# Kernel tuning notes

Hardware: AMD Instinct MI355X
Metric: run time of the kernel (lower is better)

The kernel has to match this reference:

```python
import jax, jax.numpy as jnp
import numpy as np

# config values (from init_kwargs)
TRANSFORM_PENALTY = 0.5
EXACT_MATCH_BONUS = 5.0
ULTRA_TEAL_IOU = 0.85
STRICT_MATCH_W = 0.15
CREATIVITY_W = 0.1
STRATEGIC_W = 0.1
MULTI_STEP_W = 0.1
GAMMA = 2.5
NUM_COLORS = 10


def setup_inputs() -> dict:
    key = jax.random.key(0)
    ks = jax.random.split(key, 6)
    B, C, H, W = 2048, 10, 48, 48
    return {
        "pred": jax.random.normal(ks[0], (B, C, H, W), dtype=jnp.float32),
        "strategic_features": jax.random.normal(ks[1], (B, 256), dtype=jnp.float32),
        "planning_score": jax.random.uniform(ks[2], (B,), dtype=jnp.float32),
        "reasoning_depth": jax.random.uniform(ks[3], (B,), dtype=jnp.float32),
        "targets": jax.random.randint(ks[4], (B, H, W), 0, 10, dtype=jnp.int32),
        "inputs": jax.random.randint(ks[5], (B, H, W), 0, 10, dtype=jnp.int32),
    }


def _spatial_weights(H, W, dtype):
    # weight = 1 + 0.3 * (1 - dist_from_center / max_dist), computed analytically
    cy, cx = H // 2, W // 2
    yy = jnp.arange(H, dtype=dtype)[:, None]
    xx = jnp.arange(W, dtype=dtype)[None, :]
    dist = jnp.sqrt((yy - cy) ** 2 + (xx - cx) ** 2)
    max_dist = np.sqrt((H // 2) ** 2 + (W // 2) ** 2)
    return 1.0 + 0.3 * (1.0 - dist / max_dist)  # [H, W]


def reference(pred, strategic_features, planning_score, reasoning_depth, targets, inputs):
    B, C, H, W = pred.shape
    t = targets  # label smoothing followed by argmax recovers the original indices

    # ---- enhanced strategic focal loss ----
    logp = jax.nn.log_softmax(pred, axis=1)                         # [B,C,H,W]
    ce = -jnp.take_along_axis(logp, t[:, None, :, :], axis=1)[:, 0]  # [B,H,W]
    pt = jnp.exp(-ce)
    # per-batch unique-color count (fixed small C -> loop over classes is fine)
    present = jnp.stack([jnp.any(t == c, axis=(1, 2)) for c in range(C)], axis=-1)  # [B,C]
    unique_colors = present.sum(axis=-1)                             # [B]
    # per-batch color-transition count (horizontal + vertical)
    transitions = (t[:, :, 1:] != t[:, :, :-1]).sum(axis=(1, 2)) + \
                  (t[:, 1:, :] != t[:, :-1, :]).sum(axis=(1, 2))     # [B]
    w = jnp.where(unique_colors > 4, 1.3, 1.0) * jnp.where(transitions > W, 1.2, 1.0)
    focal = jnp.mean((1.0 - pt) ** GAMMA * ce * w[:, None, None])

    # ---- ultra-teal weighted IoU + strict matches ----
    pred_idx = jnp.argmax(pred, axis=1)                              # [B,H,W]
    eq = (pred_idx == t)
    strict = jnp.all(eq, axis=(1, 2)).astype(pred.dtype)             # [B]
    sw = _spatial_weights(H, W, pred.dtype)                          # [H,W]
    weighted_iou = (eq.astype(pred.dtype) * sw).sum(axis=(1, 2)) / sw.sum()
    ultra_teal = ULTRA_TEAL_IOU * weighted_iou + STRICT_MATCH_W * strict
    exact_bonus = jnp.maximum(-ultra_teal.mean() * EXACT_MATCH_BONUS, -5.0)

    # ---- copy (transform) penalty ----
    copy = jnp.all(pred_idx == inputs, axis=(1, 2)).astype(pred.dtype)
    transform_penalty = copy.mean() * TRANSFORM_PENALTY

    # ---- optional bonuses ----
    creativity_bonus = jax.nn.sigmoid(strategic_features.mean()) * CREATIVITY_W
    strategic_bonus = planning_score.mean() * STRATEGIC_W
    multi_step_bonus = reasoning_depth.mean() * MULTI_STEP_W
    complexity_bonus = ultra_teal.mean() * (H * W / 1225.0) * 0.1    # H > 20 (static)

    total = (focal + transform_penalty + exact_bonus
             - creativity_bonus - strategic_bonus - multi_step_bonus - complexity_bonus)
    total = jnp.where(jnp.isnan(total) | jnp.isinf(total), jnp.minimum(focal, 10.0), total)
    return total
```

## Files before the change

### kernel.cpp

```cpp
#include <hip/hip_runtime.h>
#include <math.h>

#define BB 2048
#define CC 10
#define HH 48
#define WW 48
#define HWSZ (HH * WW)
#define HW4 (HWSZ / 4)
#define NTHREADS 256

__device__ __forceinline__ float wave_sum_f(float v) {
    #pragma unroll
    for (int off = 32; off > 0; off >>= 1) v += __shfl_down(v, off, 64);
    return v;
}
__device__ __forceinline__ int wave_sum_i(int v) {
    #pragma unroll
    for (int off = 32; off > 0; off >>= 1) v += __shfl_down(v, off, 64);
    return v;
}
__device__ __forceinline__ int wave_or_i(int v) {
    #pragma unroll
    for (int off = 32; off > 0; off >>= 1) v |= __shfl_down(v, off, 64);
    return v;
}

__global__ __launch_bounds__(NTHREADS) void per_batch_kernel(
    const float* __restrict__ pred,
    const float* __restrict__ sfeat,
    const int*   __restrict__ targets,
    const int*   __restrict__ inputs,
    float* __restrict__ focal_ws,
    float* __restrict__ ultra_teal_o,
    float* __restrict__ copy_o,
    float* __restrict__ sf_sum_o)
{
    __shared__ int tgt[HWSZ];
    __shared__ float rf[4][4];
    __shared__ int ri[4][4];

    const int b = blockIdx.x;
    const int tid = threadIdx.x;

    const float4* __restrict__ pb4 = (const float4*)(pred + (size_t)b * CC * HWSZ);
    const int4*   __restrict__ tb4 = (const int4*)(targets + (size_t)b * HWSZ);
    const int4*   __restrict__ ib4 = (const int4*)(inputs + (size_t)b * HWSZ);

    for (int g = tid; g < HW4; g += NTHREADS) {
        ((int4*)tgt)[g] = tb4[g];
    }
    __syncthreads();

    float focal_f = 0.f, iou_f = 0.f, sw_f = 0.f;
    int eq_cnt = 0, copy_cnt = 0, trans_cnt = 0, mask = 0;

    const float sw_scale = 0.3f / 33.9411254969543f;

    for (int g = tid; g < HW4; g += NTHREADS) {
        float chv[CC][4];
        #pragma unroll
        for (int c = 0; c < CC; ++c) {
            float4 v = pb4[c * HW4 + g];
            chv[c][0] = v.x; chv[c][1] = v.y; chv[c][2] = v.z; chv[c][3] = v.w;
        }
        int4 t4 = ((const int4*)tgt)[g];
        int4 i4 = ib4[g];
        int tj[4] = {t4.x, t4.y, t4.z, t4.w};
        int ij[4] = {i4.x, i4.y, i4.z, i4.w};

        const int y  = g / (WW / 4);
        const int x0 = (g % (WW / 4)) * 4;
        const int p0 = y * WW + x0;
        const float dy = (float)(y - 24);
        const float dy2 = dy * dy;

        #pragma unroll
        for (int j = 0; j < 4; ++j) {
            const int t = tj[j];
            mask |= (1 << t);
            const int x = x0 + j;
            if (x < WW - 1) trans_cnt += (t != tgt[p0 + j + 1]);
            if (y < HH - 1) trans_cnt += (t != tgt[p0 + j + WW]);

            float m = chv[0][j];
            int am = 0;
            float vt = (t == 0) ? chv[0][j] : 0.f;
            #pragma unroll
            for (int c = 1; c < CC; ++c) {
                float vv = chv[c][j];
                if (vv > m) { m = vv; am = c; }
                if (c == t) vt = vv;
            }
            float s = 0.f;
            #pragma unroll
            for (int c = 0; c < CC; ++c) s += __expf(chv[c][j] - m);
            const float lse = m + __logf(s);
            const float logpt = vt - lse;
            const float ce = -logpt;
            const float pt = __expf(logpt);
            const float om = fmaxf(1.f - pt, 0.f);
            focal_f += __powf(om, 2.5f) * ce;

            const bool e = (am == t);
            eq_cnt  += e;
            copy_cnt += (am == ij[j]);
            const float dx = (float)(x - 24);
            const float sw = 1.3f - sw_scale * __fsqrt_rn(dy2 + dx * dx);
            sw_f += sw;
            if (e) iou_f += sw;
        }
    }

    float sf = sfeat[(size_t)b * 256 + tid];

    focal_f = wave_sum_f(focal_f);
    iou_f   = wave_sum_f(iou_f);
    sw_f    = wave_sum_f(sw_f);
    sf      = wave_sum_f(sf);
    eq_cnt  = wave_sum_i(eq_cnt);
    copy_cnt= wave_sum_i(copy_cnt);
    trans_cnt = wave_sum_i(trans_cnt);
    mask    = wave_or_i(mask);

    const int wv = tid >> 6;
    if ((tid & 63) == 0) {
        rf[0][wv] = focal_f; rf[1][wv] = iou_f; rf[2][wv] = sw_f; rf[3][wv] = sf;
        ri[0][wv] = eq_cnt;  ri[1][wv] = copy_cnt; ri[2][wv] = trans_cnt; ri[3][wv] = mask;
    }
    __syncthreads();
    if (tid == 0) {
        float F = 0.f, I = 0.f, S = 0.f, SF = 0.f;
        int EQ = 0, CP = 0, TR = 0, MK = 0;
        #pragma unroll
        for (int i = 0; i < 4; ++i) {
            F += rf[0][i]; I += rf[1][i]; S += rf[2][i]; SF += rf[3][i];
            EQ += ri[0][i]; CP += ri[1][i]; TR += ri[2][i]; MK |= ri[3][i];
        }
        const int uniq = __popc(MK);
        const float w = ((uniq > 4) ? 1.3f : 1.0f) * ((TR > WW) ? 1.2f : 1.0f);
        const float strict = (EQ == HWSZ) ? 1.f : 0.f;
        const float ut = 0.85f * (I / S) + 0.15f * strict;
        focal_ws[b]    = F * w;
        ultra_teal_o[b] = ut;
        copy_o[b]      = (CP == HWSZ) ? 1.f : 0.f;
        sf_sum_o[b]    = SF;
    }
}

__global__ __launch_bounds__(NTHREADS) void finalize_kernel(
    const float* __restrict__ focal_ws,
    const float* __restrict__ ultra_teal,
    const float* __restrict__ copy_v,
    const float* __restrict__ sf_sum,
    const float* __restrict__ planning,
    const float* __restrict__ reasoning,
    float* __restrict__ out)
{
    __shared__ float rf[6][4];
    const int tid = threadIdx.x;
    float f = 0.f, u = 0.f, c = 0.f, s = 0.f, p = 0.f, r = 0.f;
    for (int i = tid; i < BB; i += NTHREADS) {
        f += focal_ws[i];
        u += ultra_teal[i];
        c += copy_v[i];
        s += sf_sum[i];
        p += planning[i];
        r += reasoning[i];
    }
    f = wave_sum_f(f); u = wave_sum_f(u); c = wave_sum_f(c);
    s = wave_sum_f(s); p = wave_sum_f(p); r = wave_sum_f(r);
    const int wv = tid >> 6;
    if ((tid & 63) == 0) {
        rf[0][wv] = f; rf[1][wv] = u; rf[2][wv] = c;
        rf[3][wv] = s; rf[4][wv] = p; rf[5][wv] = r;
    }
    __syncthreads();
    if (tid == 0) {
        float F = 0.f, U = 0.f, Cv = 0.f, S = 0.f, P = 0.f, R = 0.f;
        #pragma unroll
        for (int i = 0; i < 4; ++i) {
            F += rf[0][i]; U += rf[1][i]; Cv += rf[2][i];
            S += rf[3][i]; P += rf[4][i]; R += rf[5][i];
        }
        const float focal = F / (float)(BB * HWSZ);
        const float ut_mean = U / (float)BB;
        const float exact_bonus = fmaxf(-ut_mean * 5.0f, -5.0f);
        const float transform_penalty = (Cv / (float)BB) * 0.5f;
        const float sf_mean = S / (float)(BB * 256);
        const float creativity = (1.0f / (1.0f + __expf(-sf_mean))) * 0.1f;
        const float strategic = (P / (float)BB) * 0.1f;
        const float multi = (R / (float)BB) * 0.1f;
        const float complexity = ut_mean * ((float)HWSZ / 1225.0f) * 0.1f;
        float total = focal + transform_penalty + exact_bonus
                    - creativity - strategic - multi - complexity;
        if (isnan(total) || isinf(total)) total = fminf(focal, 10.0f);
        out[0] = total;
    }
}

extern "C" void kernel_launch(void* const* d_in, const int* in_sizes, int n_in,
                              void* d_out, int out_size, void* d_ws, size_t ws_size,
                              hipStream_t stream) {
    const float* pred      = (const float*)d_in[0];
    const float* sfeat     = (const float*)d_in[1];
    const float* planning  = (const float*)d_in[2];
    const float* reasoning = (const float*)d_in[3];
    const int*   targets   = (const int*)d_in[4];
    const int*   inputs    = (const int*)d_in[5];
    float* out = (float*)d_out;

    float* ws = (float*)d_ws;
    float* focal_ws   = ws;
    float* ultra_teal = ws + BB;
    float* copy_v     = ws + 2 * BB;
    float* sf_sum     = ws + 3 * BB;

    per_batch_kernel<<<BB, NTHREADS, 0, stream>>>(
        pred, sfeat, targets, inputs, focal_ws, ultra_teal, copy_v, sf_sum);
    finalize_kernel<<<1, NTHREADS, 0, stream>>>(
        focal_ws, ultra_teal, copy_v, sf_sum, planning, reasoning, out);
}
```

Measured before the change: 303.7 us.

## Rework per-batch kernel to 384 threads with float2 loads and unrolled iterations

The per-batch block grows from 256 to 384 threads, and each thread processes 2 pixels per step instead of 4, with a fully unrolled fixed trip count (3 iterations). Targets and inputs are prefetched into registers, spatial weights are precomputed into shared memory, and pow(om,2.5) becomes om*om*sqrt(om). The aim is more independent memory loads in flight and less per-pixel math on this memory-bound kernel. The trade-off is narrower 8-byte loads, which may issue more instructions per byte, plus extra shared memory and register pressure.

```diff
diff --git a/kernel.cpp b/kernel.cpp
--- a/kernel.cpp
+++ b/kernel.cpp
@@ -6,8 +6,10 @@
 #define HH 48
 #define WW 48
 #define HWSZ (HH * WW)
-#define HW4 (HWSZ / 4)
-#define NTHREADS 256
+#define HW2 (HWSZ / 2)
+#define NT 384
+#define NITER (HW2 / NT)
+#define NWAVE (NT / 64)
 
 __device__ __forceinline__ float wave_sum_f(float v) {
     #pragma unroll
@@ -25,7 +27,7 @@
     return v;
 }
 
-__global__ __launch_bounds__(NTHREADS) void per_batch_kernel(
+__global__ __launch_bounds__(NT, 4) void per_batch_kernel(
     const float* __restrict__ pred,
     const float* __restrict__ sfeat,
     const int*   __restrict__ targets,
@@ -35,96 +37,114 @@
     float* __restrict__ copy_o,
     float* __restrict__ sf_sum_o)
 {
-    __shared__ int tgt[HWSZ];
-    __shared__ float rf[4][4];
-    __shared__ int ri[4][4];
+    __shared__ int   tgt[HWSZ];
+    __shared__ float swt[HWSZ];
+    __shared__ float rf[4][NWAVE];
+    __shared__ int   ri[4][NWAVE];
 
     const int b = blockIdx.x;
     const int tid = threadIdx.x;
 
-    const float4* __restrict__ pb4 = (const float4*)(pred + (size_t)b * CC * HWSZ);
-    const int4*   __restrict__ tb4 = (const int4*)(targets + (size_t)b * HWSZ);
-    const int4*   __restrict__ ib4 = (const int4*)(inputs + (size_t)b * HWSZ);
-
-    for (int g = tid; g < HW4; g += NTHREADS) {
-        ((int4*)tgt)[g] = tb4[g];
+    const float2* __restrict__ pb2 = (const float2*)(pred + (size_t)b * CC * HWSZ);
+    const int2*   __restrict__ tb2 = (const int2*)(targets + (size_t)b * HWSZ);
+    const int2*   __restrict__ ib2 = (const int2*)(inputs + (size_t)b * HWSZ);
+
+    int2 treg[NITER], ireg[NITER];
+    #pragma unroll
+    for (int k = 0; k < NITER; ++k) {
+        const int g = tid + k * NT;
+        treg[k] = tb2[g];
+        ireg[k] = ib2[g];
+        ((int2*)tgt)[g] = treg[k];
+    }
+    const float sw_scale = 0.3f / 33.9411254969543f;
+    #pragma unroll
+    for (int k = 0; k < HWSZ / NT; ++k) {
+        const int s = tid + k * NT;
+        const int y = s / WW;
+        const int x = s - y * WW;
+        const float dy = (float)(y - 24);
+        const float dx = (float)(x - 24);
+        swt[s] = 1.3f - sw_scale * __fsqrt_rn(dy * dy + dx * dx);
     }
     __syncthreads();
 
-    float focal_f = 0.f, iou_f = 0.f, sw_f = 0.f;
+    float focal_f = 0.f, iou_f = 0.f, swsum_f = 0.f;
     int eq_cnt = 0, copy_cnt = 0, trans_cnt = 0, mask = 0;
 
-    const float sw_scale = 0.3f / 33.9411254969543f;
-
-    for (int g = tid; g < HW4; g += NTHREADS) {
-        float chv[CC][4];
+    #pragma unroll
+    for (int k = 0; k < NITER; ++k) {
+        const int g = tid + k * NT;
+        float2 v[CC];
+        #pragma unroll
+        for (int c = 0; c < CC; ++c) v[c] = pb2[c * HW2 + g];
+
+        const int2 t2 = treg[k];
+        const int2 i2 = ireg[k];
+        const int p0 = 2 * g;
+        const int y  = g / (WW / 2);
+        const int x0 = (g - y * (WW / 2)) * 2;
+
+        int th = (t2.x != t2.y);
+        if (x0 < WW - 2) th += (t2.y != tgt[p0 + 2]);
+        if (y < HH - 1) {
+            const int2 bl = ((const int2*)tgt)[g + WW / 2];
+            th += (t2.x != bl.x) + (t2.y != bl.y);
+        }
+        trans_cnt += th;
+        mask |= (1 << t2.x) | (1 << t2.y);
+
+        float m0 = v[0].x, m1 = v[0].y;
+        int a0 = 0, a1 = 0;
+        float vt0 = (t2.x == 0) ? v[0].x : 0.f;
+        float vt1 = (t2.y == 0) ? v[0].y : 0.f;
+        #pragma unroll
+        for (int c = 1; c < CC; ++c) {
+            const float vx = v[c].x, vy = v[c].y;
+            if (vx > m0) { m0 = vx; a0 = c; }
+            if (vy > m1) { m1 = vy; a1 = c; }
+            if (c == t2.x) vt0 = vx;
+            if (c == t2.y) vt1 = vy;
+        }
+        float s0 = 0.f, s1 = 0.f;
         #pragma unroll
         for (int c = 0; c < CC; ++c) {
-            float4 v = pb4[c * HW4 + g];
-            chv[c][0] = v.x; chv[c][1] = v.y; chv[c][2] = v.z; chv[c][3] = v.w;
-        }
-        int4 t4 = ((const int4*)tgt)[g];
-        int4 i4 = ib4[g];
-        int tj[4] = {t4.x, t4.y, t4.z, t4.w};
-        int ij[4] = {i4.x, i4.y, i4.z, i4.w};
-
-        const int y  = g / (WW / 4);
-        const int x0 = (g % (WW / 4)) * 4;
-        const int p0 = y * WW + x0;
-        const float dy = (float)(y - 24);
-        const float dy2 = dy * dy;
-
-        #pragma unroll
-        for (int j = 0; j < 4; ++j) {
-            const int t = tj[j];
-            mask |= (1 << t);
-            const int x = x0 + j;
-            if (x < WW - 1) trans_cnt += (t != tgt[p0 + j + 1]);
-            if (y < HH - 1) trans_cnt += (t != tgt[p0 + j + WW]);
-
-            float m = chv[0][j];
-            int am = 0;
-            float vt = (t == 0) ? chv[0][j] : 0.f;
-            #pragma unroll
-            for (int c = 1; c < CC; ++c) {
-                float vv = chv[c][j];
-                if (vv > m) { m = vv; am = c; }
-                if (c == t) vt = vv;
-            }
-            float s = 0.f;
-            #pragma unroll
-            for (int c = 0; c < CC; ++c) s += __expf(chv[c][j] - m);
-            const float lse = m + __logf(s);
-            const float logpt = vt - lse;
-            const float ce = -logpt;
-            const float pt = __expf(logpt);
-            const float om = fmaxf(1.f - pt, 0.f);
-            focal_f += __powf(om, 2.5f) * ce;
-
-            const bool e = (am == t);
-            eq_cnt  += e;
-            copy_cnt += (am == ij[j]);
-            const float dx = (float)(x - 24);
-            const float sw = 1.3f - sw_scale * __fsqrt_rn(dy2 + dx * dx);
-            sw_f += sw;
-            if (e) iou_f += sw;
-        }
-    }
-
-    float sf = sfeat[(size_t)b * 256 + tid];
-
-    focal_f = wave_sum_f(focal_f);
-    iou_f   = wave_sum_f(iou_f);
-    sw_f    = wave_sum_f(sw_f);
-    sf      = wave_sum_f(sf);
-    eq_cnt  = wave_sum_i(eq_cnt);
-    copy_cnt= wave_sum_i(copy_cnt);
+            s0 += __expf(v[c].x - m0);
+            s1 += __expf(v[c].y - m1);
+        }
+        const float lse0 = m0 + __logf(s0);
+        const float lse1 = m1 + __logf(s1);
+        const float ce0 = lse0 - vt0;
+        const float ce1 = lse1 - vt1;
+        const float pt0 = __expf(vt0 - lse0);
+        const float pt1 = __expf(vt1 - lse1);
+        const float om0 = fmaxf(1.f - pt0, 0.f);
+        const float om1 = fmaxf(1.f - pt1, 0.f);
+        focal_f += om0 * om0 * __fsqrt_rn(om0) * ce0
+                 + om1 * om1 * __fsqrt_rn(om1) * ce1;
+
+        eq_cnt   += (a0 == t2.x) + (a1 == t2.y);
+        copy_cnt += (a0 == i2.x) + (a1 == i2.y);
+
+        const float2 swp = ((const float2*)swt)[g];
+        swsum_f += swp.x + swp.y;
+        iou_f   += ((a0 == t2.x) ? swp.x : 0.f) + ((a1 == t2.y) ? swp.y : 0.f);
+    }
+
+    float sf = (tid < 256) ? sfeat[(size_t)b * 256 + tid] : 0.f;
+
+    focal_f  = wave_sum_f(focal_f);
+    iou_f    = wave_sum_f(iou_f);
+    swsum_f  = wave_sum_f(swsum_f);
+    sf       = wave_sum_f(sf);
+    eq_cnt   = wave_sum_i(eq_cnt);
+    copy_cnt = wave_sum_i(copy_cnt);
     trans_cnt = wave_sum_i(trans_cnt);
-    mask    = wave_or_i(mask);
+    mask     = wave_or_i(mask);
 
     const int wv = tid >> 6;
     if ((tid & 63) == 0) {
-        rf[0][wv] = focal_f; rf[1][wv] = iou_f; rf[2][wv] = sw_f; rf[3][wv] = sf;
+        rf[0][wv] = focal_f; rf[1][wv] = iou_f; rf[2][wv] = swsum_f; rf[3][wv] = sf;
         ri[0][wv] = eq_cnt;  ri[1][wv] = copy_cnt; ri[2][wv] = trans_cnt; ri[3][wv] = mask;
     }
     __syncthreads();
@@ -132,7 +152,7 @@
         float F = 0.f, I = 0.f, S = 0.f, SF = 0.f;
         int EQ = 0, CP = 0, TR = 0, MK = 0;
         #pragma unroll
-        for (int i = 0; i < 4; ++i) {
+        for (int i = 0; i < NWAVE; ++i) {
             F += rf[0][i]; I += rf[1][i]; S += rf[2][i]; SF += rf[3][i];
             EQ += ri[0][i]; CP += ri[1][i]; TR += ri[2][i]; MK |= ri[3][i];
         }
@@ -140,14 +160,14 @@
         const float w = ((uniq > 4) ? 1.3f : 1.0f) * ((TR > WW) ? 1.2f : 1.0f);
         const float strict = (EQ == HWSZ) ? 1.f : 0.f;
         const float ut = 0.85f * (I / S) + 0.15f * strict;
-        focal_ws[b]    = F * w;
+        focal_ws[b]     = F * w;
         ultra_teal_o[b] = ut;
-        copy_o[b]      = (CP == HWSZ) ? 1.f : 0.f;
-        sf_sum_o[b]    = SF;
-    }
-}
-
-__global__ __launch_bounds__(NTHREADS) void finalize_kernel(
+        copy_o[b]       = (CP == HWSZ) ? 1.f : 0.f;
+        sf_sum_o[b]     = SF;
+    }
+}
+
+__global__ __launch_bounds__(256) void finalize_kernel(
     const float* __restrict__ focal_ws,
     const float* __restrict__ ultra_teal,
     const float* __restrict__ copy_v,
@@ -159,7 +179,7 @@
     __shared__ float rf[6][4];
     const int tid = threadIdx.x;
     float f = 0.f, u = 0.f, c = 0.f, s = 0.f, p = 0.f, r = 0.f;
-    for (int i = tid; i < BB; i += NTHREADS) {
+    for (int i = tid; i < BB; i += 256) {
         f += focal_ws[i];
         u += ultra_teal[i];
         c += copy_v[i];
@@ -215,8 +235,8 @@
     float* copy_v     = ws + 2 * BB;
     float* sf_sum     = ws + 3 * BB;
 
-    per_batch_kernel<<<BB, NTHREADS, 0, stream>>>(
+    per_batch_kernel<<<BB, NT, 0, stream>>>(
         pred, sfeat, targets, inputs, focal_ws, ultra_teal, copy_v, sf_sum);
-    finalize_kernel<<<1, NTHREADS, 0, stream>>>(
+    finalize_kernel<<<1, 256, 0, stream>>>(
         focal_ws, ultra_teal, copy_v, sf_sum, planning, reasoning, out);
 }
```

New measurement: 296.8 us. -2.3%, faster.

## Split each batch image across three blocks with one float4 group per thread

Applied to the files above, without the earlier changes.

Each batch item is now handled by three blocks of 192 threads. Each thread loads exactly one float4 group of all ten channels up front, instead of one 256-thread block looping over 576 groups. The per-batch weighting (unique colours, transitions, strict match) moves into a 1024-thread finalize kernel that combines the three partial records per batch. This raises the number of blocks and the memory-level parallelism, and replaces powf with om*om*sqrt(om). The cost is a larger intermediate workspace and a heavier single-block finalize.

```diff
diff --git a/kernel.cpp b/kernel.cpp
--- a/kernel.cpp
+++ b/kernel.cpp
@@ -7,7 +7,10 @@
 #define WW 48
 #define HWSZ (HH * WW)
 #define HW4 (HWSZ / 4)
-#define NTHREADS 256
+#define NPART 3
+#define NT1 192
+#define GPP (HW4 / NPART)
+#define NFLD 8
 
 __device__ __forceinline__ float wave_sum_f(float v) {
     #pragma unroll
@@ -25,171 +28,181 @@
     return v;
 }
 
-__global__ __launch_bounds__(NTHREADS) void per_batch_kernel(
+__global__ __launch_bounds__(NT1) void part_kernel(
     const float* __restrict__ pred,
     const float* __restrict__ sfeat,
     const int*   __restrict__ targets,
     const int*   __restrict__ inputs,
-    float* __restrict__ focal_ws,
-    float* __restrict__ ultra_teal_o,
-    float* __restrict__ copy_o,
-    float* __restrict__ sf_sum_o)
+    float* __restrict__ ws_part)
 {
-    __shared__ int tgt[HWSZ];
-    __shared__ float rf[4][4];
-    __shared__ int ri[4][4];
-
-    const int b = blockIdx.x;
+    __shared__ int4  tgt4[GPP + WW / 4];
+    __shared__ float rf[4][3];
+    __shared__ int   ri[4][3];
+
+    const int blk = blockIdx.x;
+    const int b   = blk / NPART;
+    const int p   = blk - b * NPART;
     const int tid = threadIdx.x;
 
     const float4* __restrict__ pb4 = (const float4*)(pred + (size_t)b * CC * HWSZ);
     const int4*   __restrict__ tb4 = (const int4*)(targets + (size_t)b * HWSZ);
     const int4*   __restrict__ ib4 = (const int4*)(inputs + (size_t)b * HWSZ);
 
-    for (int g = tid; g < HW4; g += NTHREADS) {
-        ((int4*)tgt)[g] = tb4[g];
-    }
+    const int g = p * GPP + tid;
+
+    float4 v[CC];
+    #pragma unroll
+    for (int c = 0; c < CC; ++c) v[c] = pb4[c * HW4 + g];
+    const int4 t4 = tb4[g];
+    const int4 i4 = ib4[g];
+    int4 bnd = make_int4(0, 0, 0, 0);
+    const bool has_bnd = (p < NPART - 1) && (tid < WW / 4);
+    if (has_bnd) bnd = tb4[(p + 1) * GPP + tid];
+    float sf = 0.f;
+    if (p < 2 && tid < 128) sf = sfeat[(size_t)b * 256 + p * 128 + tid];
+
+    tgt4[tid] = t4;
+    if (has_bnd) tgt4[GPP + tid] = bnd;
     __syncthreads();
 
-    float focal_f = 0.f, iou_f = 0.f, sw_f = 0.f;
-    int eq_cnt = 0, copy_cnt = 0, trans_cnt = 0, mask = 0;
-
+    const int yl = tid / (WW / 4);
+    const int xg = (tid - yl * (WW / 4)) * 4;
+    const int yg = p * 16 + yl;
+
+    const int tj[4] = {t4.x, t4.y, t4.z, t4.w};
+    const int ij[4] = {i4.x, i4.y, i4.z, i4.w};
+
+    int mask = (1 << tj[0]) | (1 << tj[1]) | (1 << tj[2]) | (1 << tj[3]);
+    int tr = (tj[0] != tj[1]) + (tj[1] != tj[2]) + (tj[2] != tj[3]);
+    if (xg < WW - 4) {
+        const int* tgts = (const int*)tgt4;
+        tr += (tj[3] != tgts[(tid + 1) * 4]);
+    }
+    if (yg < HH - 1) {
+        const int4 bl = tgt4[tid + WW / 4];
+        tr += (tj[0] != bl.x) + (tj[1] != bl.y) + (tj[2] != bl.z) + (tj[3] != bl.w);
+    }
+
+    int eq = 0, cp = 0;
+    float focal = 0.f, iou = 0.f, swsum = 0.f;
     const float sw_scale = 0.3f / 33.9411254969543f;
-
-    for (int g = tid; g < HW4; g += NTHREADS) {
-        float chv[CC][4];
-        #pragma unroll
-        for (int c = 0; c < CC; ++c) {
-            float4 v = pb4[c * HW4 + g];
-            chv[c][0] = v.x; chv[c][1] = v.y; chv[c][2] = v.z; chv[c][3] = v.w;
-        }
-        int4 t4 = ((const int4*)tgt)[g];
-        int4 i4 = ib4[g];
-        int tj[4] = {t4.x, t4.y, t4.z, t4.w};
-        int ij[4] = {i4.x, i4.y, i4.z, i4.w};
-
-        const int y  = g / (WW / 4);
-        const int x0 = (g % (WW / 4)) * 4;
-        const int p0 = y * WW + x0;
-        const float dy = (float)(y - 24);
-        const float dy2 = dy * dy;
-
-        #pragma unroll
-        for (int j = 0; j < 4; ++j) {
-            const int t = tj[j];
-            mask |= (1 << t);
-            const int x = x0 + j;
-            if (x < WW - 1) trans_cnt += (t != tgt[p0 + j + 1]);
-            if (y < HH - 1) trans_cnt += (t != tgt[p0 + j + WW]);
-
-            float m = chv[0][j];
-            int am = 0;
-            float vt = (t == 0) ? chv[0][j] : 0.f;
-            #pragma unroll
-            for (int c = 1; c < CC; ++c) {
-                float vv = chv[c][j];
-                if (vv > m) { m = vv; am = c; }
-                if (c == t) vt = vv;
-            }
-            float s = 0.f;
-            #pragma unroll
-            for (int c = 0; c < CC; ++c) s += __expf(chv[c][j] - m);
-            const float lse = m + __logf(s);
-            const float logpt = vt - lse;
-            const float ce = -logpt;
-            const float pt = __expf(logpt);
-            const float om = fmaxf(1.f - pt, 0.f);
-            focal_f += __powf(om, 2.5f) * ce;
-
-            const bool e = (am == t);
-            eq_cnt  += e;
-            copy_cnt += (am == ij[j]);
-            const float dx = (float)(x - 24);
-            const float sw = 1.3f - sw_scale * __fsqrt_rn(dy2 + dx * dx);
-            sw_f += sw;
-            if (e) iou_f += sw;
-        }
-    }
-
-    float sf = sfeat[(size_t)b * 256 + tid];
-
-    focal_f = wave_sum_f(focal_f);
-    iou_f   = wave_sum_f(iou_f);
-    sw_f    = wave_sum_f(sw_f);
-    sf      = wave_sum_f(sf);
-    eq_cnt  = wave_sum_i(eq_cnt);
-    copy_cnt= wave_sum_i(copy_cnt);
-    trans_cnt = wave_sum_i(trans_cnt);
-    mask    = wave_or_i(mask);
+    const float dy = (float)(yg - 24);
+    const float dy2 = dy * dy;
+
+    #pragma unroll
+    for (int j = 0; j < 4; ++j) {
+        const float pv[4] = {0.f, 0.f, 0.f, 0.f}; (void)pv;
+        const int t = tj[j];
+        float m = (&v[0].x)[j];
+        int am = 0;
+        float vt = (t == 0) ? m : 0.f;
+        #pragma unroll
+        for (int c = 1; c < CC; ++c) {
+            const float vv = (&v[c].x)[j];
+            if (vv > m) { m = vv; am = c; }
+            if (c == t) vt = vv;
+        }
+        float s = 0.f;
+        #pragma unroll
+        for (int c = 0; c < CC; ++c) s += __expf((&v[c].x)[j] - m);
+        const float lse = m + __logf(s);
+        const float ce = lse - vt;
+        const float pt = __expf(vt - lse);
+        const float om = fmaxf(1.f - pt, 0.f);
+        focal += om * om * __fsqrt_rn(om) * ce;
+
+        const bool e = (am == t);
+        eq += e;
+        cp += (am == ij[j]);
+        const float dx = (float)(xg + j - 24);
+        const float sw = 1.3f - sw_scale * __fsqrt_rn(dy2 + dx * dx);
+        swsum += sw;
+        if (e) iou += sw;
+    }
+
+    focal = wave_sum_f(focal);
+    iou   = wave_sum_f(iou);
+    swsum = wave_sum_f(swsum);
+    sf    = wave_sum_f(sf);
+    eq    = wave_sum_i(eq);
+    cp    = wave_sum_i(cp);
+    tr    = wave_sum_i(tr);
+    mask  = wave_or_i(mask);
 
     const int wv = tid >> 6;
     if ((tid & 63) == 0) {
-        rf[0][wv] = focal_f; rf[1][wv] = iou_f; rf[2][wv] = sw_f; rf[3][wv] = sf;
-        ri[0][wv] = eq_cnt;  ri[1][wv] = copy_cnt; ri[2][wv] = trans_cnt; ri[3][wv] = mask;
+        rf[0][wv] = focal; rf[1][wv] = iou; rf[2][wv] = swsum; rf[3][wv] = sf;
+        ri[0][wv] = eq;    ri[1][wv] = cp;  ri[2][wv] = tr;    ri[3][wv] = mask;
     }
     __syncthreads();
     if (tid == 0) {
         float F = 0.f, I = 0.f, S = 0.f, SF = 0.f;
         int EQ = 0, CP = 0, TR = 0, MK = 0;
         #pragma unroll
-        for (int i = 0; i < 4; ++i) {
+        for (int i = 0; i < 3; ++i) {
             F += rf[0][i]; I += rf[1][i]; S += rf[2][i]; SF += rf[3][i];
             EQ += ri[0][i]; CP += ri[1][i]; TR += ri[2][i]; MK |= ri[3][i];
         }
-        const int uniq = __popc(MK);
-        const float w = ((uniq > 4) ? 1.3f : 1.0f) * ((TR > WW) ? 1.2f : 1.0f);
-        const float strict = (EQ == HWSZ) ? 1.f : 0.f;
-        const float ut = 0.85f * (I / S) + 0.15f * strict;
-        focal_ws[b]    = F * w;
-        ultra_teal_o[b] = ut;
-        copy_o[b]      = (CP == HWSZ) ? 1.f : 0.f;
-        sf_sum_o[b]    = SF;
-    }
-}
-
-__global__ __launch_bounds__(NTHREADS) void finalize_kernel(
-    const float* __restrict__ focal_ws,
-    const float* __restrict__ ultra_teal,
-    const float* __restrict__ copy_v,
-    const float* __restrict__ sf_sum,
+        float* q = ws_part + (size_t)(b * NPART + p) * NFLD;
+        int* qi = (int*)q;
+        q[0] = F; q[1] = I; q[2] = S; q[3] = SF;
+        qi[4] = EQ; qi[5] = CP; qi[6] = TR; qi[7] = MK;
+    }
+}
+
+__global__ __launch_bounds__(1024) void finalize_kernel(
+    const float* __restrict__ ws_part,
     const float* __restrict__ planning,
     const float* __restrict__ reasoning,
     float* __restrict__ out)
 {
-    __shared__ float rf[6][4];
+    __shared__ float rf[6][16];
     const int tid = threadIdx.x;
-    float f = 0.f, u = 0.f, c = 0.f, s = 0.f, p = 0.f, r = 0.f;
-    for (int i = tid; i < BB; i += NTHREADS) {
-        f += focal_ws[i];
-        u += ultra_teal[i];
-        c += copy_v[i];
-        s += sf_sum[i];
-        p += planning[i];
-        r += reasoning[i];
-    }
-    f = wave_sum_f(f); u = wave_sum_f(u); c = wave_sum_f(c);
-    s = wave_sum_f(s); p = wave_sum_f(p); r = wave_sum_f(r);
+
+    float F = 0.f, U = 0.f, Cv = 0.f, S = 0.f, P = 0.f, R = 0.f;
+    for (int b = tid; b < BB; b += 1024) {
+        float f = 0.f, io = 0.f, sw = 0.f, sfs = 0.f;
+        int eq = 0, cp = 0, tr = 0, mk = 0;
+        #pragma unroll
+        for (int p = 0; p < NPART; ++p) {
+            const float* q = ws_part + (size_t)(b * NPART + p) * NFLD;
+            const int* qi = (const int*)q;
+            f += q[0]; io += q[1]; sw += q[2]; sfs += q[3];
+            eq += qi[4]; cp += qi[5]; tr += qi[6]; mk |= qi[7];
+        }
+        const float w = ((__popc(mk) > 4) ? 1.3f : 1.0f) * ((tr > WW) ? 1.2f : 1.0f);
+        F += f * w;
+        const float strict = (eq == HWSZ) ? 1.f : 0.f;
+        U += 0.85f * (io / sw) + 0.15f * strict;
+        Cv += (cp == HWSZ) ? 1.f : 0.f;
+        S += sfs;
+        P += planning[b];
+        R += reasoning[b];
+    }
+
+    F = wave_sum_f(F); U = wave_sum_f(U); Cv = wave_sum_f(Cv);
+    S = wave_sum_f(S); P = wave_sum_f(P); R = wave_sum_f(R);
     const int wv = tid >> 6;
     if ((tid & 63) == 0) {
-        rf[0][wv] = f; rf[1][wv] = u; rf[2][wv] = c;
-        rf[3][wv] = s; rf[4][wv] = p; rf[5][wv] = r;
+        rf[0][wv] = F; rf[1][wv] = U; rf[2][wv] = Cv;
+        rf[3][wv] = S; rf[4][wv] = P; rf[5][wv] = R;
     }
     __syncthreads();
     if (tid == 0) {
-        float F = 0.f, U = 0.f, Cv = 0.f, S = 0.f, P = 0.f, R = 0.f;
-        #pragma unroll
-        for (int i = 0; i < 4; ++i) {
-            F += rf[0][i]; U += rf[1][i]; Cv += rf[2][i];
-            S += rf[3][i]; P += rf[4][i]; R += rf[5][i];
-        }
-        const float focal = F / (float)(BB * HWSZ);
-        const float ut_mean = U / (float)BB;
+        float Ft = 0.f, Ut = 0.f, Ct = 0.f, St = 0.f, Pt = 0.f, Rt = 0.f;
+        #pragma unroll
+        for (int i = 0; i < 16; ++i) {
+            Ft += rf[0][i]; Ut += rf[1][i]; Ct += rf[2][i];
+            St += rf[3][i]; Pt += rf[4][i]; Rt += rf[5][i];
+        }
+        const float focal = Ft / (float)(BB * HWSZ);
+        const float ut_mean = Ut / (float)BB;
         const float exact_bonus = fmaxf(-ut_mean * 5.0f, -5.0f);
-        const float transform_penalty = (Cv / (float)BB) * 0.5f;
-        const float sf_mean = S / (float)(BB * 256);
+        const float transform_penalty = (Ct / (float)BB) * 0.5f;
+        const float sf_mean = St / (float)(BB * 256);
         const float creativity = (1.0f / (1.0f + __expf(-sf_mean))) * 0.1f;
-        const float strategic = (P / (float)BB) * 0.1f;
-        const float multi = (R / (float)BB) * 0.1f;
+        const float strategic = (Pt / (float)BB) * 0.1f;
+        const float multi = (Rt / (float)BB) * 0.1f;
         const float complexity = ut_mean * ((float)HWSZ / 1225.0f) * 0.1f;
         float total = focal + transform_penalty + exact_bonus
                     - creativity - strategic - multi - complexity;
@@ -208,15 +221,10 @@
     const int*   targets   = (const int*)d_in[4];
     const int*   inputs    = (const int*)d_in[5];
     float* out = (float*)d_out;
-
-    float* ws = (float*)d_ws;
-    float* focal_ws   = ws;
-    float* ultra_teal = ws + BB;
-    float* copy_v     = ws + 2 * BB;
-    float* sf_sum     = ws + 3 * BB;
-
-    per_batch_kernel<<<BB, NTHREADS, 0, stream>>>(
-        pred, sfeat, targets, inputs, focal_ws, ultra_teal, copy_v, sf_sum);
-    finalize_kernel<<<1, NTHREADS, 0, stream>>>(
-        focal_ws, ultra_teal, copy_v, sf_sum, planning, reasoning, out);
-}
+    float* ws_part = (float*)d_ws;
+
+    part_kernel<<<BB * NPART, NT1, 0, stream>>>(
+        pred, sfeat, targets, inputs, ws_part);
+    finalize_kernel<<<1, 1024, 0, stream>>>(
+        ws_part, planning, reasoning, out);
+}
```

After: 297.7 us. 1.02x faster.
